# Performance work log

Hardware: AMD Instinct MI355X
Metric: run time of the kernel (lower is better)

Reference implementation:

```python
import jax, jax.numpy as jnp
import numpy as np


def setup_inputs() -> dict:
    key = jax.random.key(0)
    B, S, V = 4, 4096, 32000
    x = jax.random.randint(key, (B, S), 0, V, dtype=jnp.int32)
    return {"x": x, "d_vocab": V}


def reference(x, d_vocab):
    # Math identical to: gather(cumsum(one_hot(x, d_vocab), axis=1), x)
    # i.e. counts[b, s] = #{t <= s : x[b, t] == x[b, s]} (inclusive running count).
    # Implemented as an O(seq) scan over per-vocab counters instead of
    # materializing the [B, S, V] one-hot cumsum.
    B, S = x.shape
    batch_idx = jnp.arange(B)

    def step(counters, xt):  # counters: [B, V], xt: [B]
        counters = counters.at[batch_idx, xt].add(1.0)
        return counters, counters[batch_idx, xt]

    init = jnp.zeros((B, d_vocab), dtype=jnp.float32)
    _, counts = jax.lax.scan(step, init, x.T)  # counts: [S, B]
    return counts.T[..., None]  # [B, S, 1] float32, matching torch gather output
```

## Files before the change

### kernel.cpp

```cpp
#include <hip/hip_runtime.h>


#define SEQ 4096
#define QT  64
#define SL  8

__global__ __launch_bounds__(SL * 64)
void count_kernel(const int* __restrict__ x, float* __restrict__ out) {
    const int qt  = blockIdx.x;
    const int b   = blockIdx.y;
    const int tid = threadIdx.x;
    const int q   = tid & 63;
    const int g   = tid >> 6;
    const int* __restrict__ row = x + b * SEQ;

    __shared__ int prefix[SEQ];
    __shared__ int partial[SL][QT];

    const int end_i4 = (qt + 1) * (QT / 4);
    for (int j = tid; j < end_i4; j += SL * 64)
        reinterpret_cast<int4*>(prefix)[j] =
            reinterpret_cast<const int4*>(row)[j];
    __syncthreads();

    const int s    = (qt << 6) + q;
    const int qval = prefix[s];

    int c0 = 0, c1 = 0;
    const int per = qt * (16 / SL);
    const int lo  = g * per;
    const int hi  = lo + per;
    #pragma unroll 4
    for (int j = lo; j < hi; j += 2) {
        const int4 a  = reinterpret_cast<const int4*>(prefix)[j];
        const int4 a2 = reinterpret_cast<const int4*>(prefix)[j + 1];
        c0 += (qval == a.x)  + (qval == a.y)  + (qval == a.z)  + (qval == a.w);
        c1 += (qval == a2.x) + (qval == a2.y) + (qval == a2.z) + (qval == a2.w);
    }

    const int dbase = qt << 4;
    #pragma unroll
    for (int jj = 0; jj < 2; ++jj) {
        const int k = (g << 3) + (jj << 2);
        const int4 a = reinterpret_cast<const int4*>(prefix)[dbase + (k >> 2)];
        c0 += (int)((k + 0 <= q) & (qval == a.x))
            + (int)((k + 1 <= q) & (qval == a.y))
            + (int)((k + 2 <= q) & (qval == a.z))
            + (int)((k + 3 <= q) & (qval == a.w));
    }

    partial[g][q] = c0 + c1;
    __syncthreads();

    if (tid < QT) {
        int tot = 0;
        #pragma unroll
        for (int w = 0; w < SL; ++w) tot += partial[w][tid];
        out[b * SEQ + (qt << 6) + tid] = (float)tot;
    }
}

extern "C" void kernel_launch(void* const* d_in, const int* in_sizes, int n_in,
                              void* d_out, int out_size, void* d_ws, size_t ws_size,
                              hipStream_t stream) {
    const int* x = (const int*)d_in[0];
    float* out = (float*)d_out;
    const int B = in_sizes[0] / SEQ;

    count_kernel<<<dim3(SEQ / QT, B), SL * 64, 0, stream>>>(x, out);
}
```

Baseline: 59.96 us.

## Pack tokens into 16-bit pairs and count matches with packed SIMD min

New measurement: 61.85 us. 3.1% more time.

```diff
diff --git a/kernel.cpp b/kernel.cpp
--- a/kernel.cpp
+++ b/kernel.cpp
@@ -4,8 +4,15 @@
 #define SEQ 4096
 #define QT  64
 #define SL  8
+#define NT  (SL * 64)
 
-__global__ __launch_bounds__(SL * 64)
+typedef unsigned short u16x2 __attribute__((ext_vector_type(2)));
+
+static __device__ __forceinline__ u16x2 bc16(unsigned v) {
+    return __builtin_bit_cast(u16x2, v);
+}
+
+__global__ __launch_bounds__(NT)
 void count_kernel(const int* __restrict__ x, float* __restrict__ out) {
     const int qt  = blockIdx.x;
     const int b   = blockIdx.y;
@@ -14,42 +21,55 @@
     const int g   = tid >> 6;
     const int* __restrict__ row = x + b * SEQ;
 
-    __shared__ int prefix[SEQ];
+    __shared__ int pk[SEQ / 2];
+    __shared__ int diag[QT];
     __shared__ int partial[SL][QT];
 
-    const int end_i4 = (qt + 1) * (QT / 4);
-    for (int j = tid; j < end_i4; j += SL * 64)
-        reinterpret_cast<int4*>(prefix)[j] =
-            reinterpret_cast<const int4*>(row)[j];
+    const int K = qt << 6;
+
+    const int n_i4 = qt << 3;
+    for (int j = tid; j < n_i4; j += NT) {
+        const int4 g0 = reinterpret_cast<const int4*>(row)[2 * j];
+        const int4 g1 = reinterpret_cast<const int4*>(row)[2 * j + 1];
+        int4 p;
+        p.x = (int)(((unsigned)g0.x) | ((unsigned)g0.y << 16));
+        p.y = (int)(((unsigned)g0.z) | ((unsigned)g0.w << 16));
+        p.z = (int)(((unsigned)g1.x) | ((unsigned)g1.y << 16));
+        p.w = (int)(((unsigned)g1.z) | ((unsigned)g1.w << 16));
+        reinterpret_cast<int4*>(pk)[j] = p;
+    }
+    if (tid < QT) diag[tid] = row[K + tid];
     __syncthreads();
 
-    const int s    = (qt << 6) + q;
-    const int qval = prefix[s];
+    const int      qval = diag[q];
+    const unsigned qpk  = ((unsigned)qval) | ((unsigned)qval << 16);
+    const u16x2    one  = {1, 1};
 
-    int c0 = 0, c1 = 0;
-    const int per = qt * (16 / SL);
-    const int lo  = g * per;
-    const int hi  = lo + per;
+    u16x2 m0 = {0, 0}, m1 = {0, 0};
+    const int lo = g * qt;
+    const int hi = lo + qt;
     #pragma unroll 4
-    for (int j = lo; j < hi; j += 2) {
-        const int4 a  = reinterpret_cast<const int4*>(prefix)[j];
-        const int4 a2 = reinterpret_cast<const int4*>(prefix)[j + 1];
-        c0 += (qval == a.x)  + (qval == a.y)  + (qval == a.z)  + (qval == a.w);
-        c1 += (qval == a2.x) + (qval == a2.y) + (qval == a2.z) + (qval == a2.w);
+    for (int j = lo; j < hi; ++j) {
+        const int4 a = reinterpret_cast<const int4*>(pk)[j];
+        m0 += __builtin_elementwise_min(bc16(qpk ^ (unsigned)a.x), one);
+        m1 += __builtin_elementwise_min(bc16(qpk ^ (unsigned)a.y), one);
+        m0 += __builtin_elementwise_min(bc16(qpk ^ (unsigned)a.z), one);
+        m1 += __builtin_elementwise_min(bc16(qpk ^ (unsigned)a.w), one);
     }
+    int cnt = (qt << 3) - (int)((unsigned)m0.x + (unsigned)m0.y
+                             + (unsigned)m1.x + (unsigned)m1.y);
 
-    const int dbase = qt << 4;
     #pragma unroll
     for (int jj = 0; jj < 2; ++jj) {
         const int k = (g << 3) + (jj << 2);
-        const int4 a = reinterpret_cast<const int4*>(prefix)[dbase + (k >> 2)];
-        c0 += (int)((k + 0 <= q) & (qval == a.x))
-            + (int)((k + 1 <= q) & (qval == a.y))
-            + (int)((k + 2 <= q) & (qval == a.z))
-            + (int)((k + 3 <= q) & (qval == a.w));
+        const int4 a = reinterpret_cast<const int4*>(diag)[k >> 2];
+        cnt += (int)((k + 0 <= q) & (qval == a.x))
+             + (int)((k + 1 <= q) & (qval == a.y))
+             + (int)((k + 2 <= q) & (qval == a.z))
+             + (int)((k + 3 <= q) & (qval == a.w));
     }
 
-    partial[g][q] = c0 + c1;
+    partial[g][q] = cnt;
     __syncthreads();
 
     if (tid < QT) {
@@ -67,5 +87,5 @@
     float* out = (float*)d_out;
     const int B = in_sizes[0] / SEQ;
 
-    count_kernel<<<dim3(SEQ / QT, B), SL * 64, 0, stream>>>(x, out);
+    count_kernel<<<dim3(SEQ / QT, B), NT, 0, stream>>>(x, out);
 }
```
